# Optimization experiments

Measured on AMD Instinct MI355X. Metric: run time of the kernel, lower is better.

## Reference

```python
import jax, jax.numpy as jnp
import numpy as np

N_EVENT, N_IOC = 10000, 40000
N = N_EVENT + N_IOC
E = 800000
D_EVENT, D_IOC = 768, 128
H = 256            # hidden_dim
R = 8              # num_relations
B = 8              # num_bases
L = 3              # num_layers
EDIM = 16          # edge_type_embed_dim
LN_EPS = 1e-5


def setup_inputs() -> dict:
    key = jax.random.key(0)
    ks = jax.random.split(key, 24)
    inp = {}
    inp['x_event'] = jax.random.normal(ks[0], (N_EVENT, D_EVENT), dtype=jnp.float32)
    inp['x_ioc'] = jax.random.normal(ks[1], (N_IOC, D_IOC), dtype=jnp.float32)
    inp['edge_index'] = jax.random.randint(ks[2], (2, E), 0, N, dtype=jnp.int32)
    inp['edge_type'] = jax.random.randint(ks[3], (E,), 0, R, dtype=jnp.int32)
    inp['edge_weight'] = jax.random.uniform(ks[4], (E,), dtype=jnp.float32)
    # input projection params (Linear + LayerNorm per node type)
    inp['proj_event_w'] = jax.random.normal(ks[5], (D_EVENT, H), dtype=jnp.float32) / np.sqrt(D_EVENT)
    inp['proj_event_b'] = jnp.zeros((H,), jnp.float32)
    inp['proj_event_g'] = jnp.ones((H,), jnp.float32)
    inp['proj_event_beta'] = jnp.zeros((H,), jnp.float32)
    inp['proj_ioc_w'] = jax.random.normal(ks[6], (D_IOC, H), dtype=jnp.float32) / np.sqrt(D_IOC)
    inp['proj_ioc_b'] = jnp.zeros((H,), jnp.float32)
    inp['proj_ioc_g'] = jnp.ones((H,), jnp.float32)
    inp['proj_ioc_beta'] = jnp.zeros((H,), jnp.float32)
    # edge-type embedding + edge MLP
    inp['edge_emb'] = jax.random.normal(ks[7], (R, EDIM), dtype=jnp.float32)
    inp['edge_mlp_w'] = jax.random.normal(ks[8], (EDIM + 1, H), dtype=jnp.float32) / np.sqrt(EDIM + 1)
    inp['edge_mlp_b'] = jnp.zeros((H,), jnp.float32)
    # RGCN layers: basis-decomposed relation weights + root + bias, per-layer LayerNorm
    inp['conv_bases'] = jax.random.normal(ks[9], (L, B, H, H), dtype=jnp.float32) / np.sqrt(H)
    inp['conv_comp'] = jax.random.normal(ks[10], (L, R, B), dtype=jnp.float32) / np.sqrt(B)
    inp['conv_root'] = jax.random.normal(ks[11], (L, H, H), dtype=jnp.float32) / np.sqrt(H)
    inp['conv_bias'] = jnp.zeros((L, H), jnp.float32)
    inp['norm_gamma'] = jnp.ones((L, H), jnp.float32)
    inp['norm_beta'] = jnp.zeros((L, H), jnp.float32)
    return inp


def _ln(x, g, b):
    mu = jnp.mean(x, axis=-1, keepdims=True)
    var = jnp.var(x, axis=-1, keepdims=True)
    return (x - mu) * jax.lax.rsqrt(var + LN_EPS) * g + b


def reference(x_event, x_ioc, edge_index, edge_type, edge_weight,
              proj_event_w, proj_event_b, proj_event_g, proj_event_beta,
              proj_ioc_w, proj_ioc_b, proj_ioc_g, proj_ioc_beta,
              edge_emb, edge_mlp_w, edge_mlp_b,
              conv_bases, conv_comp, conv_root, conv_bias,
              norm_gamma, norm_beta):
    # input projections: Linear -> LayerNorm -> ReLU, then concat EVENT first
    h_ev = jax.nn.relu(_ln(x_event @ proj_event_w + proj_event_b, proj_event_g, proj_event_beta))
    h_io = jax.nn.relu(_ln(x_ioc @ proj_ioc_w + proj_ioc_b, proj_ioc_g, proj_ioc_beta))
    h = jnp.concatenate([h_ev, h_io], axis=0)  # [N, H]
    n, d = h.shape
    src, dst = edge_index[0], edge_index[1]
    r = edge_emb.shape[0]

    # edge-feature MLP (edge_type embedding ++ weight), eval mode so dropout is identity
    ef = jnp.concatenate([edge_emb[edge_type], edge_weight[:, None]], axis=-1)  # [E, EDIM+1]
    enh = jax.nn.relu(ef @ edge_mlp_w + edge_mlp_b)                              # [E, H]
    enh_sum = jax.ops.segment_sum(enh, dst, num_segments=n)
    deg = jax.ops.segment_sum(jnp.ones(enh.shape[0], h.dtype), dst, num_segments=n)
    enh_mean = enh_sum / jnp.maximum(deg, 1.0)[:, None]                           # [N, H]

    ones_e = jnp.ones(src.shape[0], h.dtype)
    seg = dst.astype(jnp.int32) * r + edge_type                                   # per-(dst, relation) segments
    cnt = jnp.maximum(jax.ops.segment_sum(ones_e, seg, num_segments=n * r), 1.0)

    for l in range(conv_bases.shape[0]):
        # basis-decomposed relation weights: W_r = sum_b comp[r,b] * basis_b
        w = jnp.einsum('rb,bio->rio', conv_comp[l], conv_bases[l])   # [R, H, H]
        xr = jnp.einsum('ni,rio->rno', h, w)                          # [R, N, H]
        msg = xr[edge_type, src]                                      # [E, H]
        # per-relation mean aggregation per destination node (PyG RGCNConv aggr='mean')
        sums = jax.ops.segment_sum(msg, seg, num_segments=n * r)      # [N*R, H]
        agg = (sums / cnt[:, None]).reshape(n, r, d).sum(axis=1)      # [N, H]
        h_new = agg + h @ conv_root[l] + conv_bias[l] + 0.1 * enh_mean
        h_new = jax.nn.relu(_ln(h_new, norm_gamma[l], norm_beta[l]))
        h = h_new + h

    return h[:x_event.shape[0]]  # EVENT node embeddings
```

## Files before the change

### kernel.cpp

```cpp
#include <hip/hip_runtime.h>
#include <hip/hip_bf16.h>

#define N_EVENT 10000
#define N_IOC   40000
#define N_NODES 50000
#define E_EDGES 800000
#define D_EV 768
#define D_IO 128
#define H 256
#define R 8
#define NBASES 8
#define NLAYERS 3
#define EDIM 16
#define LN_EPS 1e-5f

#define NKEY (N_NODES * R)
#define SCAN_CHUNK 2048
#define NCHUNK ((NKEY + SCAN_CHUNK - 1) / SCAN_CHUNK)
#define NC 12500
#define NCHUNKS (N_NODES / NC)
#define KPRE (R * H)
#define KTOT (R * H + H)
#define NBLK_EV ((N_EVENT + 63) / 64)
#define NBLK_IO (N_IOC / 64)

typedef __hip_bfloat16 bf16;
typedef __attribute__((ext_vector_type(8))) short bf16x8;
typedef __attribute__((ext_vector_type(4))) float f32x4;

__device__ __forceinline__ float us2f(unsigned short u) {
    union { unsigned int i; float f; } x; x.i = ((unsigned int)u) << 16; return x.f;
}

__global__ __launch_bounds__(256) void hist_kernel(const int* __restrict__ ei, const int* __restrict__ et,
                                                   int* __restrict__ cnt) {
    int e = blockIdx.x * 256 + threadIdx.x;
    if (e < E_EDGES) atomicAdd(&cnt[ei[E_EDGES + e] * R + et[e]], 1);
}

__global__ __launch_bounds__(256) void scan1_kernel(const int* __restrict__ cnt, int* __restrict__ offs,
                                                    int* __restrict__ bsum) {
    __shared__ int s[256];
    int t = threadIdx.x;
    long base = (long)blockIdx.x * SCAN_CHUNK + t * 8;
    int v[8]; int sum = 0;
    #pragma unroll
    for (int i = 0; i < 8; ++i) { long idx = base + i; v[i] = (idx < NKEY) ? cnt[idx] : 0; sum += v[i]; }
    s[t] = sum; __syncthreads();
    for (int off = 1; off < 256; off <<= 1) {
        int x = (t >= off) ? s[t - off] : 0;
        __syncthreads();
        s[t] += x;
        __syncthreads();
    }
    int run = s[t] - sum;
    if (t == 255) bsum[blockIdx.x] = s[255];
    #pragma unroll
    for (int i = 0; i < 8; ++i) { long idx = base + i; if (idx < NKEY) offs[idx] = run; run += v[i]; }
}

__global__ __launch_bounds__(256) void scan2_kernel(int* __restrict__ bsum) {
    __shared__ int s[256];
    int t = threadIdx.x;
    int v = (t < NCHUNK) ? bsum[t] : 0;
    s[t] = v; __syncthreads();
    for (int off = 1; off < 256; off <<= 1) {
        int x = (t >= off) ? s[t - off] : 0;
        __syncthreads();
        s[t] += x;
        __syncthreads();
    }
    if (t < NCHUNK) bsum[t] = s[t] - v;
}

__global__ __launch_bounds__(256) void scan3_kernel(int* __restrict__ offs, const int* __restrict__ bsum) {
    int i = blockIdx.x * 256 + threadIdx.x;
    if (i < NKEY) offs[i] += bsum[i / SCAN_CHUNK];
    if (i == 0) offs[NKEY] = E_EDGES;
}

__global__ __launch_bounds__(256) void cinv_kernel(const int* __restrict__ cnt, float* __restrict__ cinv) {
    int i = blockIdx.x * 256 + threadIdx.x;
    if (i < NKEY) cinv[i] = 1.0f / (float)max(cnt[i], 1);
}

__global__ __launch_bounds__(256) void sort_kernel(const int* __restrict__ ei, const int* __restrict__ et,
                                                   const float* __restrict__ ew, const int* __restrict__ offs,
                                                   int* __restrict__ cnt, int* __restrict__ ssrc,
                                                   float* __restrict__ sew) {
    int e = blockIdx.x * 256 + threadIdx.x;
    if (e >= E_EDGES) return;
    int key = ei[E_EDGES + e] * R + et[e];
    int pos = offs[key] + atomicSub(&cnt[key], 1) - 1;
    ssrc[pos] = ei[e];
    sew[pos]  = ew[e];
}

__global__ __launch_bounds__(256) void cvt_x_kernel(const float* __restrict__ xev, const float* __restrict__ xio,
                                                    bf16* __restrict__ xevb, bf16* __restrict__ xiob) {
    const long NEV4 = (long)N_EVENT * D_EV / 4;
    const long NTOT4 = NEV4 + (long)N_IOC * D_IO / 4;
    long i = (long)blockIdx.x * 256 + threadIdx.x;
    if (i >= NTOT4) return;
    const float4* src; ushort4* dst; long j;
    if (i < NEV4) { src = (const float4*)xev; dst = (ushort4*)xevb; j = i; }
    else          { src = (const float4*)xio; dst = (ushort4*)xiob; j = i - NEV4; }
    float4 v = src[j];
    ushort4 o;
    bf16 a0 = __float2bfloat16(v.x), a1 = __float2bfloat16(v.y);
    bf16 a2 = __float2bfloat16(v.z), a3 = __float2bfloat16(v.w);
    o.x = *(unsigned short*)&a0; o.y = *(unsigned short*)&a1;
    o.z = *(unsigned short*)&a2; o.w = *(unsigned short*)&a3;
    dst[j] = o;
}

__global__ __launch_bounds__(256) void cvt_w_kernel(const float* __restrict__ wev, const float* __restrict__ wio,
                                                    bf16* __restrict__ wevT, bf16* __restrict__ wioT) {
    int n = blockIdx.x;
    for (int k = threadIdx.x; k < D_EV; k += 256)
        wevT[(size_t)n * D_EV + k] = __float2bfloat16(wev[(size_t)k * H + n]);
    for (int k = threadIdx.x; k < D_IO; k += 256)
        wioT[(size_t)n * D_IO + k] = __float2bfloat16(wio[(size_t)k * H + n]);
}

__global__ __launch_bounds__(256) void build_Bt_kernel(
    const float* __restrict__ bases, const float* __restrict__ comp, const float* __restrict__ root,
    bf16* __restrict__ Bt3) {
    int gb = blockIdx.x;
    int l = gb / KTOT, krow = gb % KTOT;
    int n = threadIdx.x;
    float v;
    if (krow < KPRE) {
        int r = krow >> 8, kk = krow & 255;
        v = 0.0f;
        const float* bs = bases + (size_t)l * NBASES * H * H + (size_t)kk * H + n;
        const float* cp = comp + (l * R + r) * NBASES;
        #pragma unroll
        for (int b = 0; b < NBASES; ++b) v += cp[b] * bs[(size_t)b * H * H];
    } else {
        int kk = krow - KPRE;
        v = root[((size_t)l * H + kk) * H + n];
    }
    Bt3[(size_t)l * H * KTOT + (size_t)n * KTOT + krow] = __float2bfloat16(v);
}

__global__ __launch_bounds__(256) void edge_table_kernel(
    const float* __restrict__ emb, const float* __restrict__ mlp_w,
    const float* __restrict__ mlp_b, float* __restrict__ ctab, float* __restrict__ wlast) {
    int r = blockIdx.x, j = threadIdx.x;
    float acc = mlp_b[j];
    #pragma unroll
    for (int k = 0; k < EDIM; ++k) acc += emb[r * EDIM + k] * mlp_w[k * H + j];
    ctab[r * H + j] = acc;
    if (r == 0) wlast[j] = mlp_w[EDIM * H + j];
}

__global__ __launch_bounds__(256) void enh_bucket_kernel(
    const int* __restrict__ offs, const float* __restrict__ sew,
    const float* __restrict__ ctab, const float* __restrict__ wlast,
    bf16* __restrict__ enh) {
    __shared__ float ct[R * H];
    __shared__ float wl[H];
    for (int i = threadIdx.x; i < R * H; i += 256) ct[i] = ctab[i];
    for (int i = threadIdx.x; i < H; i += 256) wl[i] = wlast[i];
    __syncthreads();
    int w = threadIdx.x >> 6, lane = threadIdx.x & 63;
    int d = blockIdx.x * 4 + w;
    float acc[4] = {0.f, 0.f, 0.f, 0.f};
    int deg = offs[d * R + R] - offs[d * R];
    for (int r = 0; r < R; ++r) {
        int a = offs[d * R + r], b = offs[d * R + r + 1];
        for (int j = a; j < b; ++j) {
            float wt = sew[j];
            #pragma unroll
            for (int i = 0; i < 4; ++i) {
                int c = lane * 4 + i;
                acc[i] += fmaxf(ct[r * H + c] + wt * wl[c], 0.0f);
            }
        }
    }
    float inv = 1.0f / fmaxf((float)deg, 1.0f);
    unsigned short o[4];
    #pragma unroll
    for (int i = 0; i < 4; ++i) { bf16 hv = __float2bfloat16(acc[i] * inv); o[i] = *(unsigned short*)&hv; }
    *(ushort4*)(enh + (size_t)d * H + lane * 4) = *(ushort4*)o;
}

__global__ __launch_bounds__(256) void bucket_msg_kernel(
    const int* __restrict__ offs, const int* __restrict__ ssrc,
    const bf16* __restrict__ hbR, const float* __restrict__ cinv,
    bf16* __restrict__ pre, int c0) {
    int w = threadIdx.x >> 6, lane = threadIdx.x & 63;
    int d = c0 + blockIdx.x;
    size_t prow = (size_t)blockIdx.x * KPRE;
    #pragma unroll
    for (int rr = 0; rr < 2; ++rr) {
        int r = w * 2 + rr;
        float acc[4] = {0.f, 0.f, 0.f, 0.f};
        int a = offs[d * R + r], b = offs[d * R + r + 1];
        for (int j = a; j < b; ++j) {
            int s = ssrc[j];
            ushort4 u = *(const ushort4*)(hbR + (size_t)s * H + lane * 4);
            acc[0] += us2f(u.x); acc[1] += us2f(u.y); acc[2] += us2f(u.z); acc[3] += us2f(u.w);
        }
        float sc = cinv[d * R + r];
        unsigned short o[4];
        #pragma unroll
        for (int i = 0; i < 4; ++i) { bf16 hv = __float2bfloat16(acc[i] * sc); o[i] = *(unsigned short*)&hv; }
        *(ushort4*)(pre + prow + r * H + lane * 4) = *(ushort4*)o;
    }
}

__global__ __launch_bounds__(256) void gemm_ln_kernel(
    const bf16* __restrict__ pre, const bf16* __restrict__ hbR,
    const bf16* __restrict__ Bt, const bf16* __restrict__ enh,
    const float* __restrict__ bias, const float* __restrict__ gamma, const float* __restrict__ beta,
    float* __restrict__ h, bf16* __restrict__ hbW, int c0) {
    __shared__ bf16 bts[256 * 40];
    int t = threadIdx.x, w = t >> 6, lane = t & 63;
    int quad = lane >> 4, m = lane & 15;
    int rowbase = blockIdx.x * 64 + w * 16;
    f32x4 acc[16];
    #pragma unroll
    for (int c = 0; c < 16; ++c) { acc[c][0] = 0.f; acc[c][1] = 0.f; acc[c][2] = 0.f; acc[c][3] = 0.f; }
    int rowA = rowbase + m;
    int rA = (rowA < NC) ? rowA : (NC - 1);
    const bf16* Apre = pre + (size_t)rA * KPRE;
    const bf16* Ahb  = hbR + (size_t)(c0 + rA) * H;

    for (int kc = 0; kc < KTOT / 32; ++kc) {
        int k0 = kc * 32;
        {
            const bf16* g = Bt + (size_t)t * KTOT + k0;
            bf16* l = bts + t * 40;
            *(bf16x8*)(l + 0)  = *(const bf16x8*)(g + 0);
            *(bf16x8*)(l + 8)  = *(const bf16x8*)(g + 8);
            *(bf16x8*)(l + 16) = *(const bf16x8*)(g + 16);
            *(bf16x8*)(l + 24) = *(const bf16x8*)(g + 24);
        }
        bf16x8 a;
        if (k0 < KPRE) a = *(const bf16x8*)(Apre + k0 + quad * 8);
        else           a = *(const bf16x8*)(Ahb + (k0 - KPRE) + quad * 8);
        __syncthreads();
        #pragma unroll
        for (int c = 0; c < 16; ++c) {
            bf16x8 b = *(const bf16x8*)(bts + (c * 16 + m) * 40 + quad * 8);
            acc[c] = __builtin_amdgcn_mfma_f32_16x16x32_bf16(a, b, acc[c], 0, 0, 0);
        }
        __syncthreads();
    }

    float bv[16], gv[16], tv[16];
    #pragma unroll
    for (int c = 0; c < 16; ++c) {
        int col = c * 16 + m;
        bv[c] = bias[col]; gv[c] = gamma[col]; tv[c] = beta[col];
    }
    float s[4] = {0.f,0.f,0.f,0.f}, s2[4] = {0.f,0.f,0.f,0.f};
    #pragma unroll
    for (int c = 0; c < 16; ++c) {
        #pragma unroll
        for (int i = 0; i < 4; ++i) {
            int row = rowbase + quad * 4 + i;
            int rr = (row < NC) ? row : (NC - 1);
            float e = us2f(*(const unsigned short*)(enh + (size_t)(c0 + rr) * H + c * 16 + m));
            float val = acc[c][i] + bv[c] + 0.1f * e;
            acc[c][i] = val;
            s[i] += val; s2[i] += val * val;
        }
    }
    #pragma unroll
    for (int msk = 1; msk < 16; msk <<= 1) {
        #pragma unroll
        for (int i = 0; i < 4; ++i) { s[i] += __shfl_xor(s[i], msk); s2[i] += __shfl_xor(s2[i], msk); }
    }
    float mu[4], rstd[4];
    #pragma unroll
    for (int i = 0; i < 4; ++i) {
        mu[i] = s[i] * (1.0f / H);
        float var = s2[i] * (1.0f / H) - mu[i] * mu[i];
        rstd[i] = rsqrtf(var + LN_EPS);
    }
    #pragma unroll
    for (int c = 0; c < 16; ++c) {
        #pragma unroll
        for (int i = 0; i < 4; ++i) {
            int row = rowbase + quad * 4 + i;
            if (row < NC) {
                size_t idx = (size_t)(c0 + row) * H + c * 16 + m;
                float y = (acc[c][i] - mu[i]) * rstd[i] * gv[c] + tv[c];
                float hn = h[idx] + fmaxf(y, 0.0f);
                h[idx] = hn;
                hbW[idx] = __float2bfloat16(hn);
            }
        }
    }
}

__global__ __launch_bounds__(256) void proj_gemm_kernel(
    const bf16* __restrict__ xevb, const bf16* __restrict__ xiob,
    const bf16* __restrict__ wevT, const bf16* __restrict__ wioT,
    const float* __restrict__ bev, const float* __restrict__ gev, const float* __restrict__ betev,
    const float* __restrict__ bio, const float* __restrict__ gio, const float* __restrict__ betio,
    float* __restrict__ h, bf16* __restrict__ hbW) {
    __shared__ bf16 bts[256 * 40];
    int t = threadIdx.x, w = t >> 6, lane = t & 63;
    int quad = lane >> 4, m = lane & 15;
    int blk = blockIdx.x;
    const bf16 *X, *WT; const float *bb, *gg, *be;
    int K, node0, x0, nvalid;
    if (blk < NBLK_EV) {
        X = xevb; WT = wevT; K = D_EV; node0 = blk * 64; x0 = node0;
        bb = bev; gg = gev; be = betev;
        nvalid = (N_EVENT - node0 < 64) ? (N_EVENT - node0) : 64;
    } else {
        int b2 = blk - NBLK_EV;
        X = xiob; WT = wioT; K = D_IO; node0 = N_EVENT + b2 * 64; x0 = b2 * 64;
        bb = bio; gg = gio; be = betio;
        nvalid = 64;
    }
    int rowbase = w * 16;
    f32x4 acc[16];
    #pragma unroll
    for (int c = 0; c < 16; ++c) { acc[c][0] = 0.f; acc[c][1] = 0.f; acc[c][2] = 0.f; acc[c][3] = 0.f; }
    int rowA = rowbase + m;
    int rA = (rowA < nvalid) ? rowA : (nvalid - 1);
    const bf16* Ax = X + (size_t)(x0 + rA) * K;

    for (int kc = 0; kc < K / 32; ++kc) {
        int k0 = kc * 32;
        {
            const bf16* g = WT + (size_t)t * K + k0;
            bf16* l = bts + t * 40;
            *(bf16x8*)(l + 0)  = *(const bf16x8*)(g + 0);
            *(bf16x8*)(l + 8)  = *(const bf16x8*)(g + 8);
            *(bf16x8*)(l + 16) = *(const bf16x8*)(g + 16);
            *(bf16x8*)(l + 24) = *(const bf16x8*)(g + 24);
        }
        bf16x8 a = *(const bf16x8*)(Ax + k0 + quad * 8);
        __syncthreads();
        #pragma unroll
        for (int c = 0; c < 16; ++c) {
            bf16x8 b = *(const bf16x8*)(bts + (c * 16 + m) * 40 + quad * 8);
            acc[c] = __builtin_amdgcn_mfma_f32_16x16x32_bf16(a, b, acc[c], 0, 0, 0);
        }
        __syncthreads();
    }

    float bv[16], gv[16], tv[16];
    #pragma unroll
    for (int c = 0; c < 16; ++c) {
        int col = c * 16 + m;
        bv[c] = bb[col]; gv[c] = gg[col]; tv[c] = be[col];
    }
    float s[4] = {0.f,0.f,0.f,0.f}, s2[4] = {0.f,0.f,0.f,0.f};
    #pragma unroll
    for (int c = 0; c < 16; ++c) {
        #pragma unroll
        for (int i = 0; i < 4; ++i) {
            float val = acc[c][i] + bv[c];
            acc[c][i] = val;
            s[i] += val; s2[i] += val * val;
        }
    }
    #pragma unroll
    for (int msk = 1; msk < 16; msk <<= 1) {
        #pragma unroll
        for (int i = 0; i < 4; ++i) { s[i] += __shfl_xor(s[i], msk); s2[i] += __shfl_xor(s2[i], msk); }
    }
    float mu[4], rstd[4];
    #pragma unroll
    for (int i = 0; i < 4; ++i) {
        mu[i] = s[i] * (1.0f / H);
        float var = s2[i] * (1.0f / H) - mu[i] * mu[i];
        rstd[i] = rsqrtf(var + LN_EPS);
    }
    #pragma unroll
    for (int c = 0; c < 16; ++c) {
        #pragma unroll
        for (int i = 0; i < 4; ++i) {
            int row = rowbase + quad * 4 + i;
            if (row < nvalid) {
                size_t idx = (size_t)(node0 + row) * H + c * 16 + m;
                float y = (acc[c][i] - mu[i]) * rstd[i] * gv[c] + tv[c];
                float hn = fmaxf(y, 0.0f);
                h[idx] = hn;
                hbW[idx] = __float2bfloat16(hn);
            }
        }
    }
}

extern "C" void kernel_launch(void* const* d_in, const int* in_sizes, int n_in,
                              void* d_out, int out_size, void* d_ws, size_t ws_size,
                              hipStream_t stream) {
    const float* xev   = (const float*)d_in[0];
    const float* xio   = (const float*)d_in[1];
    const int*   ei    = (const int*)d_in[2];
    const int*   et    = (const int*)d_in[3];
    const float* ew    = (const float*)d_in[4];
    const float* wev   = (const float*)d_in[5];
    const float* bev   = (const float*)d_in[6];
    const float* gev   = (const float*)d_in[7];
    const float* betev = (const float*)d_in[8];
    const float* wio   = (const float*)d_in[9];
    const float* bio   = (const float*)d_in[10];
    const float* gio   = (const float*)d_in[11];
    const float* betio = (const float*)d_in[12];
    const float* emb   = (const float*)d_in[13];
    const float* mlp_w = (const float*)d_in[14];
    const float* mlp_b = (const float*)d_in[15];
    const float* bases = (const float*)d_in[16];
    const float* comp  = (const float*)d_in[17];
    const float* root  = (const float*)d_in[18];
    const float* bias  = (const float*)d_in[19];
    const float* gamma = (const float*)d_in[20];
    const float* beta  = (const float*)d_in[21];

    char* base = (char*)d_ws;
    size_t o = 0;
    auto alloc = [&](size_t bytes) { char* p = base + o; o = (o + bytes + 255) & ~(size_t)255; return p; };
    float* h    = (float*)alloc((size_t)N_NODES * H * 4);
    bf16*  hbA  = (bf16*) alloc((size_t)N_NODES * H * 2);
    bf16*  hbB  = (bf16*) alloc((size_t)N_NODES * H * 2);
    bf16*  enh  = (bf16*) alloc((size_t)N_NODES * H * 2);
    char*  un   = alloc((size_t)NC * KPRE * 2);
    bf16*  pre  = (bf16*)un;
    bf16*  xevb = (bf16*)un;
    bf16*  xiob = (bf16*)(un + (size_t)N_EVENT * D_EV * 2);
    bf16*  wevT = (bf16*) alloc((size_t)H * D_EV * 2);
    bf16*  wioT = (bf16*) alloc((size_t)H * D_IO * 2);
    bf16*  Bt3  = (bf16*) alloc((size_t)NLAYERS * H * KTOT * 2);
    float* ctab = (float*)alloc(R * H * 4);
    float* wlast= (float*)alloc(H * 4);
    float* cinv = (float*)alloc((size_t)NKEY * 4);
    int*   bsum = (int*)  alloc(256 * 4);
    int*   cnt  = (int*)  alloc((size_t)NKEY * 4);
    int*   offs = (int*)  alloc((size_t)(NKEY + 4) * 4);
    int*   ssrc = (int*)  alloc((size_t)E_EDGES * 4);
    float* sew  = (float*)alloc((size_t)E_EDGES * 4);

    hipMemsetAsync(cnt, 0, (size_t)NKEY * sizeof(int), stream);

    hist_kernel<<<(E_EDGES + 255) / 256, 256, 0, stream>>>(ei, et, cnt);
    scan1_kernel<<<NCHUNK, 256, 0, stream>>>(cnt, offs, bsum);
    scan2_kernel<<<1, 256, 0, stream>>>(bsum);
    scan3_kernel<<<(NKEY + 255) / 256, 256, 0, stream>>>(offs, bsum);
    cinv_kernel<<<(NKEY + 255) / 256, 256, 0, stream>>>(cnt, cinv);
    sort_kernel<<<(E_EDGES + 255) / 256, 256, 0, stream>>>(ei, et, ew, offs, cnt, ssrc, sew);

    cvt_x_kernel<<<12500, 256, 0, stream>>>(xev, xio, xevb, xiob);
    cvt_w_kernel<<<H, 256, 0, stream>>>(wev, wio, wevT, wioT);
    build_Bt_kernel<<<NLAYERS * KTOT, 256, 0, stream>>>(bases, comp, root, Bt3);

    proj_gemm_kernel<<<NBLK_EV + NBLK_IO, 256, 0, stream>>>(
        xevb, xiob, wevT, wioT, bev, gev, betev, bio, gio, betio, h, hbA);
    edge_table_kernel<<<R, 256, 0, stream>>>(emb, mlp_w, mlp_b, ctab, wlast);
    enh_bucket_kernel<<<N_NODES / 4, 256, 0, stream>>>(offs, sew, ctab, wlast, enh);

    for (int l = 0; l < NLAYERS; ++l) {
        bf16* hbR = (l & 1) ? hbB : hbA;
        bf16* hbW = (l & 1) ? hbA : hbB;
        const bf16* Bt = Bt3 + (size_t)l * H * KTOT;
        for (int c = 0; c < NCHUNKS; ++c) {
            int c0 = c * NC;
            bucket_msg_kernel<<<NC, 256, 0, stream>>>(offs, ssrc, hbR, cinv, pre, c0);
            gemm_ln_kernel<<<(NC + 63) / 64, 256, 0, stream>>>(
                pre, hbR, Bt, enh, bias + l * H, gamma + l * H, beta + l * H, h, hbW, c0);
        }
    }

    hipMemcpyAsync(d_out, h, (size_t)N_EVENT * H * sizeof(float), hipMemcpyDeviceToDevice, stream);
}
```

Before: 2.275 ms.

## Use single-wave 32-row GEMM tiles without LDS and drop fp32 residual state

```diff
diff --git a/kernel.cpp b/kernel.cpp
--- a/kernel.cpp
+++ b/kernel.cpp
@@ -21,8 +21,8 @@
 #define NCHUNKS (N_NODES / NC)
 #define KPRE (R * H)
 #define KTOT (R * H + H)
-#define NBLK_EV ((N_EVENT + 63) / 64)
-#define NBLK_IO (N_IOC / 64)
+#define NBEV32 ((N_EVENT + 31) / 32)
+#define NBIO32 (N_IOC / 32)
 
 typedef __hip_bfloat16 bf16;
 typedef __attribute__((ext_vector_type(8))) short bf16x8;
@@ -211,43 +211,46 @@
     }
 }
 
-__global__ __launch_bounds__(256) void gemm_ln_kernel(
+__global__ __launch_bounds__(64) void gemm2_kernel(
     const bf16* __restrict__ pre, const bf16* __restrict__ hbR,
     const bf16* __restrict__ Bt, const bf16* __restrict__ enh,
     const float* __restrict__ bias, const float* __restrict__ gamma, const float* __restrict__ beta,
-    float* __restrict__ h, bf16* __restrict__ hbW, int c0) {
-    __shared__ bf16 bts[256 * 40];
-    int t = threadIdx.x, w = t >> 6, lane = t & 63;
+    bf16* __restrict__ hbW, int c0) {
+    int lane = threadIdx.x;
     int quad = lane >> 4, m = lane & 15;
-    int rowbase = blockIdx.x * 64 + w * 16;
-    f32x4 acc[16];
-    #pragma unroll
-    for (int c = 0; c < 16; ++c) { acc[c][0] = 0.f; acc[c][1] = 0.f; acc[c][2] = 0.f; acc[c][3] = 0.f; }
-    int rowA = rowbase + m;
-    int rA = (rowA < NC) ? rowA : (NC - 1);
-    const bf16* Apre = pre + (size_t)rA * KPRE;
-    const bf16* Ahb  = hbR + (size_t)(c0 + rA) * H;
-
+    int row0 = blockIdx.x * 32;
+    f32x4 acc0[16], acc1[16];
+    #pragma unroll
+    for (int c = 0; c < 16; ++c) {
+        acc0[c][0]=0.f; acc0[c][1]=0.f; acc0[c][2]=0.f; acc0[c][3]=0.f;
+        acc1[c][0]=0.f; acc1[c][1]=0.f; acc1[c][2]=0.f; acc1[c][3]=0.f;
+    }
+    int rA0 = row0 + m;      if (rA0 >= NC) rA0 = NC - 1;
+    int rA1 = row0 + 16 + m; if (rA1 >= NC) rA1 = NC - 1;
+    const bf16* A0p = pre + (size_t)rA0 * KPRE;
+    const bf16* A1p = pre + (size_t)rA1 * KPRE;
+    const bf16* A0h = hbR + (size_t)(c0 + rA0) * H;
+    const bf16* A1h = hbR + (size_t)(c0 + rA1) * H;
+    const bf16* Bbase = Bt + (size_t)m * KTOT;
+
+    #pragma unroll 2
     for (int kc = 0; kc < KTOT / 32; ++kc) {
         int k0 = kc * 32;
-        {
-            const bf16* g = Bt + (size_t)t * KTOT + k0;
-            bf16* l = bts + t * 40;
-            *(bf16x8*)(l + 0)  = *(const bf16x8*)(g + 0);
-            *(bf16x8*)(l + 8)  = *(const bf16x8*)(g + 8);
-            *(bf16x8*)(l + 16) = *(const bf16x8*)(g + 16);
-            *(bf16x8*)(l + 24) = *(const bf16x8*)(g + 24);
-        }
-        bf16x8 a;
-        if (k0 < KPRE) a = *(const bf16x8*)(Apre + k0 + quad * 8);
-        else           a = *(const bf16x8*)(Ahb + (k0 - KPRE) + quad * 8);
-        __syncthreads();
+        bf16x8 a0, a1;
+        if (k0 < KPRE) {
+            a0 = *(const bf16x8*)(A0p + k0 + quad * 8);
+            a1 = *(const bf16x8*)(A1p + k0 + quad * 8);
+        } else {
+            a0 = *(const bf16x8*)(A0h + (k0 - KPRE) + quad * 8);
+            a1 = *(const bf16x8*)(A1h + (k0 - KPRE) + quad * 8);
+        }
+        const bf16* bp = Bbase + k0 + quad * 8;
         #pragma unroll
         for (int c = 0; c < 16; ++c) {
-            bf16x8 b = *(const bf16x8*)(bts + (c * 16 + m) * 40 + quad * 8);
-            acc[c] = __builtin_amdgcn_mfma_f32_16x16x32_bf16(a, b, acc[c], 0, 0, 0);
-        }
-        __syncthreads();
+            bf16x8 b = *(const bf16x8*)(bp + (size_t)c * 16 * KTOT);
+            acc0[c] = __builtin_amdgcn_mfma_f32_16x16x32_bf16(a0, b, acc0[c], 0, 0, 0);
+            acc1[c] = __builtin_amdgcn_mfma_f32_16x16x32_bf16(a1, b, acc1[c], 0, 0, 0);
+        }
     }
 
     float bv[16], gv[16], tv[16];
@@ -256,95 +259,106 @@
         int col = c * 16 + m;
         bv[c] = bias[col]; gv[c] = gamma[col]; tv[c] = beta[col];
     }
-    float s[4] = {0.f,0.f,0.f,0.f}, s2[4] = {0.f,0.f,0.f,0.f};
+    float s0[4]={0,0,0,0}, q0[4]={0,0,0,0}, s1[4]={0,0,0,0}, q1[4]={0,0,0,0};
     #pragma unroll
     for (int c = 0; c < 16; ++c) {
         #pragma unroll
         for (int i = 0; i < 4; ++i) {
-            int row = rowbase + quad * 4 + i;
-            int rr = (row < NC) ? row : (NC - 1);
-            float e = us2f(*(const unsigned short*)(enh + (size_t)(c0 + rr) * H + c * 16 + m));
-            float val = acc[c][i] + bv[c] + 0.1f * e;
-            acc[c][i] = val;
-            s[i] += val; s2[i] += val * val;
+            int r0 = row0 + quad * 4 + i;        int rr0 = (r0 < NC) ? r0 : (NC - 1);
+            int r1 = row0 + 16 + quad * 4 + i;   int rr1 = (r1 < NC) ? r1 : (NC - 1);
+            int col = c * 16 + m;
+            float e0 = us2f(*(const unsigned short*)(enh + (size_t)(c0 + rr0) * H + col));
+            float e1 = us2f(*(const unsigned short*)(enh + (size_t)(c0 + rr1) * H + col));
+            float v0 = acc0[c][i] + bv[c] + 0.1f * e0;
+            float v1 = acc1[c][i] + bv[c] + 0.1f * e1;
+            acc0[c][i] = v0; acc1[c][i] = v1;
+            s0[i] += v0; q0[i] += v0 * v0;
+            s1[i] += v1; q1[i] += v1 * v1;
         }
     }
     #pragma unroll
     for (int msk = 1; msk < 16; msk <<= 1) {
         #pragma unroll
-        for (int i = 0; i < 4; ++i) { s[i] += __shfl_xor(s[i], msk); s2[i] += __shfl_xor(s2[i], msk); }
-    }
-    float mu[4], rstd[4];
+        for (int i = 0; i < 4; ++i) {
+            s0[i] += __shfl_xor(s0[i], msk); q0[i] += __shfl_xor(q0[i], msk);
+            s1[i] += __shfl_xor(s1[i], msk); q1[i] += __shfl_xor(q1[i], msk);
+        }
+    }
+    float mu0[4], rs0[4], mu1[4], rs1[4];
     #pragma unroll
     for (int i = 0; i < 4; ++i) {
-        mu[i] = s[i] * (1.0f / H);
-        float var = s2[i] * (1.0f / H) - mu[i] * mu[i];
-        rstd[i] = rsqrtf(var + LN_EPS);
+        mu0[i] = s0[i] * (1.0f / H);
+        rs0[i] = rsqrtf(q0[i] * (1.0f / H) - mu0[i] * mu0[i] + LN_EPS);
+        mu1[i] = s1[i] * (1.0f / H);
+        rs1[i] = rsqrtf(q1[i] * (1.0f / H) - mu1[i] * mu1[i] + LN_EPS);
     }
     #pragma unroll
     for (int c = 0; c < 16; ++c) {
         #pragma unroll
         for (int i = 0; i < 4; ++i) {
-            int row = rowbase + quad * 4 + i;
-            if (row < NC) {
-                size_t idx = (size_t)(c0 + row) * H + c * 16 + m;
-                float y = (acc[c][i] - mu[i]) * rstd[i] * gv[c] + tv[c];
-                float hn = h[idx] + fmaxf(y, 0.0f);
-                h[idx] = hn;
+            int col = c * 16 + m;
+            int r0 = row0 + quad * 4 + i;
+            if (r0 < NC) {
+                size_t idx = (size_t)(c0 + r0) * H + col;
+                float y = (acc0[c][i] - mu0[i]) * rs0[i] * gv[c] + tv[c];
+                float hn = us2f(*(const unsigned short*)(hbR + idx)) + fmaxf(y, 0.0f);
                 hbW[idx] = __float2bfloat16(hn);
             }
-        }
-    }
-}
-
-__global__ __launch_bounds__(256) void proj_gemm_kernel(
+            int r1 = row0 + 16 + quad * 4 + i;
+            if (r1 < NC) {
+                size_t idx = (size_t)(c0 + r1) * H + col;
+                float y = (acc1[c][i] - mu1[i]) * rs1[i] * gv[c] + tv[c];
+                float hn = us2f(*(const unsigned short*)(hbR + idx)) + fmaxf(y, 0.0f);
+                hbW[idx] = __float2bfloat16(hn);
+            }
+        }
+    }
+}
+
+__global__ __launch_bounds__(64) void proj2_kernel(
     const bf16* __restrict__ xevb, const bf16* __restrict__ xiob,
     const bf16* __restrict__ wevT, const bf16* __restrict__ wioT,
     const float* __restrict__ bev, const float* __restrict__ gev, const float* __restrict__ betev,
     const float* __restrict__ bio, const float* __restrict__ gio, const float* __restrict__ betio,
-    float* __restrict__ h, bf16* __restrict__ hbW) {
-    __shared__ bf16 bts[256 * 40];
-    int t = threadIdx.x, w = t >> 6, lane = t & 63;
+    bf16* __restrict__ hbW) {
+    int lane = threadIdx.x;
     int quad = lane >> 4, m = lane & 15;
     int blk = blockIdx.x;
     const bf16 *X, *WT; const float *bb, *gg, *be;
     int K, node0, x0, nvalid;
-    if (blk < NBLK_EV) {
-        X = xevb; WT = wevT; K = D_EV; node0 = blk * 64; x0 = node0;
+    if (blk < NBEV32) {
+        X = xevb; WT = wevT; K = D_EV; x0 = blk * 32; node0 = x0;
         bb = bev; gg = gev; be = betev;
-        nvalid = (N_EVENT - node0 < 64) ? (N_EVENT - node0) : 64;
+        nvalid = (N_EVENT - x0 < 32) ? (N_EVENT - x0) : 32;
     } else {
-        int b2 = blk - NBLK_EV;
-        X = xiob; WT = wioT; K = D_IO; node0 = N_EVENT + b2 * 64; x0 = b2 * 64;
+        int b2 = blk - NBEV32;
+        X = xiob; WT = wioT; K = D_IO; x0 = b2 * 32; node0 = N_EVENT + x0;
         bb = bio; gg = gio; be = betio;
-        nvalid = 64;
-    }
-    int rowbase = w * 16;
-    f32x4 acc[16];
-    #pragma unroll
-    for (int c = 0; c < 16; ++c) { acc[c][0] = 0.f; acc[c][1] = 0.f; acc[c][2] = 0.f; acc[c][3] = 0.f; }
-    int rowA = rowbase + m;
-    int rA = (rowA < nvalid) ? rowA : (nvalid - 1);
-    const bf16* Ax = X + (size_t)(x0 + rA) * K;
+        nvalid = 32;
+    }
+    f32x4 acc0[16], acc1[16];
+    #pragma unroll
+    for (int c = 0; c < 16; ++c) {
+        acc0[c][0]=0.f; acc0[c][1]=0.f; acc0[c][2]=0.f; acc0[c][3]=0.f;
+        acc1[c][0]=0.f; acc1[c][1]=0.f; acc1[c][2]=0.f; acc1[c][3]=0.f;
+    }
+    int rA0 = m;      if (rA0 >= nvalid) rA0 = nvalid - 1;
+    int rA1 = 16 + m; if (rA1 >= nvalid) rA1 = nvalid - 1;
+    const bf16* A0 = X + (size_t)(x0 + rA0) * K;
+    const bf16* A1 = X + (size_t)(x0 + rA1) * K;
+    const bf16* Bbase = WT + (size_t)m * K;
 
     for (int kc = 0; kc < K / 32; ++kc) {
         int k0 = kc * 32;
-        {
-            const bf16* g = WT + (size_t)t * K + k0;
-            bf16* l = bts + t * 40;
-            *(bf16x8*)(l + 0)  = *(const bf16x8*)(g + 0);
-            *(bf16x8*)(l + 8)  = *(const bf16x8*)(g + 8);
-            *(bf16x8*)(l + 16) = *(const bf16x8*)(g + 16);
-            *(bf16x8*)(l + 24) = *(const bf16x8*)(g + 24);
-        }
-        bf16x8 a = *(const bf16x8*)(Ax + k0 + quad * 8);
-        __syncthreads();
+        bf16x8 a0 = *(const bf16x8*)(A0 + k0 + quad * 8);
+        bf16x8 a1 = *(const bf16x8*)(A1 + k0 + quad * 8);
+        const bf16* bp = Bbase + k0 + quad * 8;
         #pragma unroll
         for (int c = 0; c < 16; ++c) {
-            bf16x8 b = *(const bf16x8*)(bts + (c * 16 + m) * 40 + quad * 8);
-            acc[c] = __builtin_amdgcn_mfma_f32_16x16x32_bf16(a, b, acc[c], 0, 0, 0);
-        }
-        __syncthreads();
+            bf16x8 b = *(const bf16x8*)(bp + (size_t)c * 16 * K);
+            acc0[c] = __builtin_amdgcn_mfma_f32_16x16x32_bf16(a0, b, acc0[c], 0, 0, 0);
+            acc1[c] = __builtin_amdgcn_mfma_f32_16x16x32_bf16(a1, b, acc1[c], 0, 0, 0);
+        }
     }
 
     float bv[16], gv[16], tv[16];
@@ -353,42 +367,56 @@
         int col = c * 16 + m;
         bv[c] = bb[col]; gv[c] = gg[col]; tv[c] = be[col];
     }
-    float s[4] = {0.f,0.f,0.f,0.f}, s2[4] = {0.f,0.f,0.f,0.f};
+    float s0[4]={0,0,0,0}, q0[4]={0,0,0,0}, s1[4]={0,0,0,0}, q1[4]={0,0,0,0};
     #pragma unroll
     for (int c = 0; c < 16; ++c) {
         #pragma unroll
         for (int i = 0; i < 4; ++i) {
-            float val = acc[c][i] + bv[c];
-            acc[c][i] = val;
-            s[i] += val; s2[i] += val * val;
+            float v0 = acc0[c][i] + bv[c];
+            float v1 = acc1[c][i] + bv[c];
+            acc0[c][i] = v0; acc1[c][i] = v1;
+            s0[i] += v0; q0[i] += v0 * v0;
+            s1[i] += v1; q1[i] += v1 * v1;
         }
     }
     #pragma unroll
     for (int msk = 1; msk < 16; msk <<= 1) {
         #pragma unroll
-        for (int i = 0; i < 4; ++i) { s[i] += __shfl_xor(s[i], msk); s2[i] += __shfl_xor(s2[i], msk); }
-    }
-    float mu[4], rstd[4];
+        for (int i = 0; i < 4; ++i) {
+            s0[i] += __shfl_xor(s0[i], msk); q0[i] += __shfl_xor(q0[i], msk);
+            s1[i] += __shfl_xor(s1[i], msk); q1[i] += __shfl_xor(q1[i], msk);
+        }
+    }
+    float mu0[4], rs0[4], mu1[4], rs1[4];
     #pragma unroll
     for (int i = 0; i < 4; ++i) {
-        mu[i] = s[i] * (1.0f / H);
-        float var = s2[i] * (1.0f / H) - mu[i] * mu[i];
-        rstd[i] = rsqrtf(var + LN_EPS);
+        mu0[i] = s0[i] * (1.0f / H);
+        rs0[i] = rsqrtf(q0[i] * (1.0f / H) - mu0[i] * mu0[i] + LN_EPS);
+        mu1[i] = s1[i] * (1.0f / H);
+        rs1[i] = rsqrtf(q1[i] * (1.0f / H) - mu1[i] * mu1[i] + LN_EPS);
     }
     #pragma unroll
     for (int c = 0; c < 16; ++c) {
         #pragma unroll
         for (int i = 0; i < 4; ++i) {
-            int row = rowbase + quad * 4 + i;
-            if (row < nvalid) {
-                size_t idx = (size_t)(node0 + row) * H + c * 16 + m;
-                float y = (acc[c][i] - mu[i]) * rstd[i] * gv[c] + tv[c];
-                float hn = fmaxf(y, 0.0f);
-                h[idx] = hn;
-                hbW[idx] = __float2bfloat16(hn);
+            int col = c * 16 + m;
+            int r0 = quad * 4 + i;
+            if (r0 < nvalid) {
+                float y = (acc0[c][i] - mu0[i]) * rs0[i] * gv[c] + tv[c];
+                hbW[(size_t)(node0 + r0) * H + col] = __float2bfloat16(fmaxf(y, 0.0f));
             }
-        }
-    }
+            int r1 = 16 + quad * 4 + i;
+            if (r1 < nvalid) {
+                float y = (acc1[c][i] - mu1[i]) * rs1[i] * gv[c] + tv[c];
+                hbW[(size_t)(node0 + r1) * H + col] = __float2bfloat16(fmaxf(y, 0.0f));
+            }
+        }
+    }
+}
+
+__global__ __launch_bounds__(256) void out_kernel(const bf16* __restrict__ hb, float* __restrict__ out) {
+    size_t i = (size_t)blockIdx.x * 256 + threadIdx.x;
+    if (i < (size_t)N_EVENT * H) out[i] = us2f(*(const unsigned short*)(hb + i));
 }
 
 extern "C" void kernel_launch(void* const* d_in, const int* in_sizes, int n_in,
@@ -420,7 +448,6 @@
     char* base = (char*)d_ws;
     size_t o = 0;
     auto alloc = [&](size_t bytes) { char* p = base + o; o = (o + bytes + 255) & ~(size_t)255; return p; };
-    float* h    = (float*)alloc((size_t)N_NODES * H * 4);
     bf16*  hbA  = (bf16*) alloc((size_t)N_NODES * H * 2);
     bf16*  hbB  = (bf16*) alloc((size_t)N_NODES * H * 2);
     bf16*  enh  = (bf16*) alloc((size_t)N_NODES * H * 2);
@@ -453,8 +480,8 @@
     cvt_w_kernel<<<H, 256, 0, stream>>>(wev, wio, wevT, wioT);
     build_Bt_kernel<<<NLAYERS * KTOT, 256, 0, stream>>>(bases, comp, root, Bt3);
 
-    proj_gemm_kernel<<<NBLK_EV + NBLK_IO, 256, 0, stream>>>(
-        xevb, xiob, wevT, wioT, bev, gev, betev, bio, gio, betio, h, hbA);
+    proj2_kernel<<<NBEV32 + NBIO32, 64, 0, stream>>>(
+        xevb, xiob, wevT, wioT, bev, gev, betev, bio, gio, betio, hbA);
     edge_table_kernel<<<R, 256, 0, stream>>>(emb, mlp_w, mlp_b, ctab, wlast);
     enh_bucket_kernel<<<N_NODES / 4, 256, 0, stream>>>(offs, sew, ctab, wlast, enh);
 
@@ -465,10 +492,10 @@
         for (int c = 0; c < NCHUNKS; ++c) {
             int c0 = c * NC;
             bucket_msg_kernel<<<NC, 256, 0, stream>>>(offs, ssrc, hbR, cinv, pre, c0);
-            gemm_ln_kernel<<<(NC + 63) / 64, 256, 0, stream>>>(
-                pre, hbR, Bt, enh, bias + l * H, gamma + l * H, beta + l * H, h, hbW, c0);
-        }
-    }
-
-    hipMemcpyAsync(d_out, h, (size_t)N_EVENT * H * sizeof(float), hipMemcpyDeviceToDevice, stream);
-}
+            gemm2_kernel<<<(NC + 31) / 32, 64, 0, stream>>>(
+                pre, hbR, Bt, enh, bias + l * H, gamma + l * H, beta + l * H, hbW, c0);
+        }
+    }
+
+    out_kernel<<<((size_t)N_EVENT * H + 255) / 256, 256, 0, stream>>>(hbB, (float*)d_out);
+}
```

After: 2.848 ms. +25.2%, slower.
